# Kernel optimization log

Hardware: AMD Instinct MI355X
Metric: run time of the kernel (lower is better)

The kernel has to match this reference:

```python
import jax, jax.numpy as jnp
import numpy as np

WH, WW = 16, 16          # window size
S = WH * WW              # tokens per window = 256
B = 128                  # batch of windows
E = 1024                 # embed_dim
H = 16                   # num_heads
D = E // H               # head_dim = 64


def _swin_rel_index():
    # Swin-style relative position index, identical to the torch buffer construction
    coords = np.stack(np.meshgrid(np.arange(WH), np.arange(WW), indexing='ij'))  # [2,WH,WW]
    cf = coords.reshape(2, -1)                         # [2, S]
    rel = cf[:, :, None] - cf[:, None, :]              # [2, S, S]
    rel = rel.transpose(1, 2, 0).copy()                # [S, S, 2]
    rel[..., 0] += WH - 1
    rel[..., 1] += WW - 1
    rel[..., 0] *= 2 * WW - 1
    return rel.sum(-1).astype(np.int32)                # [S, S] in [0, (2WH-1)(2WW-1))


def setup_inputs() -> dict:
    key = jax.random.key(0)
    ks = jax.random.split(key, 6)
    x = jax.random.normal(ks[0], (B, S, E), dtype=jnp.float32)
    qkv_w = jax.random.normal(ks[1], (3 * E, E), dtype=jnp.float32) * 0.02
    qkv_b = jax.random.normal(ks[2], (3 * E,), dtype=jnp.float32) * 0.02
    out_w = jax.random.normal(ks[3], (E, E), dtype=jnp.float32) * 0.02
    out_b = jax.random.normal(ks[4], (E,), dtype=jnp.float32) * 0.02
    bias_table = jax.random.normal(ks[5], ((2 * WH - 1) * (2 * WW - 1), H), dtype=jnp.float32) * 0.02
    rel_index = jnp.asarray(_swin_rel_index())
    return {"x": x, "qkv_w": qkv_w, "qkv_b": qkv_b, "out_w": out_w,
            "out_b": out_b, "bias_table": bias_table, "rel_index": rel_index,
            "x_ignored_": 0, "x_ignored_1_": 0}


def reference(x, qkv_w, qkv_b, out_w, out_b, bias_table, rel_index, x_ignored_, x_ignored_1_):
    b, s, e = x.shape
    h = bias_table.shape[-1]
    d = e // h
    # fused QKV projection
    qkv = x @ qkv_w.T + qkv_b                          # [b, s, 3e]
    qkv = qkv.reshape(b, s, 3, h, d)
    q, k, v = qkv[:, :, 0], qkv[:, :, 1], qkv[:, :, 2]  # [b, s, h, d]
    scale = d ** -0.5
    # learned relative position bias, [h, s, s]
    bias = bias_table[rel_index.reshape(-1)].reshape(s, s, h).transpose(2, 0, 1)
    scores = jnp.einsum('bqhd,bkhd->bhqk', q, k) * scale + bias[None]
    attn = jax.nn.softmax(scores, axis=-1)
    ctx = jnp.einsum('bhqk,bkhd->bqhd', attn, v).reshape(b, s, e)
    return ctx @ out_w.T + out_b
```

## Files before the change

kernel.cpp:

```cpp
#include <hip/hip_runtime.h>
#include <stdint.h>

#define BB 128
#define SS 256
#define EE 1024
#define HH 16
#define DD 64
#define MM (BB*SS)

#define LOG2E 1.44269504088896f

typedef __attribute__((ext_vector_type(8))) short bf16x8;
typedef __attribute__((ext_vector_type(4))) float f32x4;

__device__ __forceinline__ unsigned short f2bf(float f) {
  union { float f; unsigned int u; } c; c.f = f;
  unsigned int u = c.u;
  u += 0x7fffu + ((u >> 16) & 1u);
  return (unsigned short)(u >> 16);
}

__device__ __forceinline__ float fast_exp2(float x) {
#if __has_builtin(__builtin_amdgcn_exp2f)
  return __builtin_amdgcn_exp2f(x);
#else
  return exp2f(x);
#endif
}

__device__ __forceinline__ float fast_rcp(float x) {
#if __has_builtin(__builtin_amdgcn_rcpf)
  return __builtin_amdgcn_rcpf(x);
#else
  return 1.0f / x;
#endif
}

__device__ __forceinline__ void gld16(const unsigned short* g, unsigned short* l) {
  __builtin_amdgcn_global_load_lds((__attribute__((address_space(1))) void*)(g),
                                   (__attribute__((address_space(3))) void*)(l), 16, 0, 0);
}

__global__ __launch_bounds__(256) void prep_kernel(const float4* __restrict__ x4,
                                                   const float4* __restrict__ qw,
                                                   const float4* __restrict__ ow,
                                                   const float* __restrict__ btab,
                                                   const int* __restrict__ ridx,
                                                   ushort4* __restrict__ xb,
                                                   ushort4* __restrict__ qwb,
                                                   ushort4* __restrict__ owb,
                                                   float* __restrict__ biasC) {
  const int NX = (MM * EE) / 4;
  const int NQ = (3 * EE * EE) / 4;
  const int NO = (EE * EE) / 4;
  const int NBIAS = HH * SS * SS;
  const int total = NX + NQ + NO + NBIAS;
  int stride = gridDim.x * blockDim.x;
  for (int i = blockIdx.x * blockDim.x + threadIdx.x; i < total; i += stride) {
    if (i < NX) {
      float4 v = x4[i];
      ushort4 r; r.x = f2bf(v.x); r.y = f2bf(v.y); r.z = f2bf(v.z); r.w = f2bf(v.w);
      xb[i] = r;
    } else if (i < NX + NQ) {
      int t = i - NX;
      float4 v = qw[t];
      ushort4 r; r.x = f2bf(v.x); r.y = f2bf(v.y); r.z = f2bf(v.z); r.w = f2bf(v.w);
      qwb[t] = r;
    } else if (i < NX + NQ + NO) {
      int t = i - (NX + NQ);
      float4 v = ow[t];
      ushort4 r; r.x = f2bf(v.x); r.y = f2bf(v.y); r.z = f2bf(v.z); r.w = f2bf(v.w);
      owb[t] = r;
    } else {
      int t = i - (NX + NQ + NO);
      int h   = t >> 16;
      int row = (t >> 8) & 255;
      int lo  = (t >> 4) & 15;
      int hi  = t & 15;
      int col = hi * 16 + lo;
      biasC[t] = btab[ridx[row * SS + col] * HH + h] * LOG2E;
    }
  }
}

__device__ __forceinline__ void gemm_mainloop(const unsigned short* __restrict__ A,
                                              const unsigned short* __restrict__ Bw,
                                              unsigned short* As, unsigned short* Bs,
                                              int row0, int col0, int K,
                                              f32x4 acc[4][4]) {
  const int tid = threadIdx.x;
  const int wave = tid >> 6, lane = tid & 63;
  const int wm = wave & 1, wn = wave >> 1;
  const int l15 = lane & 15, quad = lane >> 4;
  const int ldrow = lane >> 2, ldc = lane & 3;
  const int gsw = (ldc ^ ((ldrow >> 1) & 3)) * 8;
  const int rsw = (l15 >> 1) & 3;
  const unsigned short* agp0 = A + (size_t)(row0 + wave * 16 + ldrow) * K + gsw;
  const unsigned short* agp1 = A + (size_t)(row0 + (4 + wave) * 16 + ldrow) * K + gsw;
  const unsigned short* bgp0 = Bw + (size_t)(col0 + wave * 16 + ldrow) * K + gsw;
  const unsigned short* bgp1 = Bw + (size_t)(col0 + (4 + wave) * 16 + ldrow) * K + gsw;
  unsigned short* al0 = As + wave * 512;
  unsigned short* al1 = As + (4 + wave) * 512;
  unsigned short* bl0 = Bs + wave * 512;
  unsigned short* bl1 = Bs + (4 + wave) * 512;
  for (int k0 = 0; k0 < K; k0 += 32) {
    gld16(agp0 + k0, al0);
    gld16(agp1 + k0, al1);
    gld16(bgp0 + k0, bl0);
    gld16(bgp1 + k0, bl1);
    __syncthreads();
    bf16x8 af[4], bfm[4];
#pragma unroll
    for (int i = 0; i < 4; ++i)
      af[i] = *(const bf16x8*)(As + (wm * 64 + i * 16 + l15) * 32 + (quad ^ rsw) * 8);
#pragma unroll
    for (int j = 0; j < 4; ++j)
      bfm[j] = *(const bf16x8*)(Bs + (wn * 64 + j * 16 + l15) * 32 + (quad ^ rsw) * 8);
#pragma unroll
    for (int i = 0; i < 4; ++i)
#pragma unroll
      for (int j = 0; j < 4; ++j)
        acc[i][j] = __builtin_amdgcn_mfma_f32_16x16x32_bf16(af[i], bfm[j], acc[i][j], 0, 0, 0);
    __syncthreads();
  }
}

__global__ __launch_bounds__(256) void qkv_gemm(const unsigned short* __restrict__ A,
                                                const unsigned short* __restrict__ Bw,
                                                const float* __restrict__ bias,
                                                unsigned short* __restrict__ q,
                                                unsigned short* __restrict__ kx,
                                                unsigned short* __restrict__ vt) {
  __shared__ unsigned short As[128 * 32];
  __shared__ unsigned short Bs[128 * 32];
  const int tid = threadIdx.x;
  const int wave = tid >> 6, lane = tid & 63;
  const int wm = wave & 1, wn = wave >> 1;
  const int l15 = lane & 15, quad = lane >> 4;
  const int row0 = blockIdx.x * 128;
  const int col0 = blockIdx.y * 128;
  f32x4 acc[4][4];
#pragma unroll
  for (int i = 0; i < 4; ++i)
#pragma unroll
    for (int j = 0; j < 4; ++j) acc[i][j] = (f32x4){0.f, 0.f, 0.f, 0.f};
  gemm_mainloop(A, Bw, As, Bs, row0, col0, EE, acc);
  const int which = col0 >> 10;
  const float QS = 0.125f * LOG2E;
#pragma unroll
  for (int i = 0; i < 4; ++i) {
    const int mbase = row0 + wm * 64 + i * 16 + quad * 4;
    const int bb = mbase >> 8;
    const int s0 = mbase & 255;
#pragma unroll
    for (int j = 0; j < 4; ++j) {
      const int n = col0 + wn * 64 + j * 16 + l15;
      const int hn = (n >> 6) & 15;
      const int d = n & 63;
      const float bv = bias[n];
      if (which == 0) {
        size_t base = ((size_t)(bb * HH + hn) * SS + s0) * DD + d;
#pragma unroll
        for (int r = 0; r < 4; ++r)
          q[base + (size_t)r * DD] = f2bf((acc[i][j][r] + bv) * QS);
      } else if (which == 1) {
        size_t base = ((size_t)(bb * HH + hn) * SS + s0) * DD + d;
#pragma unroll
        for (int r = 0; r < 4; ++r)
          kx[base + (size_t)r * DD] = f2bf(acc[i][j][r] + bv);
      } else {
        size_t base = ((size_t)(bb * HH + hn) * DD + d) * SS + s0;
        ushort4 pk;
        pk.x = f2bf(acc[i][j][0] + bv);
        pk.y = f2bf(acc[i][j][1] + bv);
        pk.z = f2bf(acc[i][j][2] + bv);
        pk.w = f2bf(acc[i][j][3] + bv);
        *(ushort4*)(vt + base) = pk;
      }
    }
  }
}

__global__ __launch_bounds__(256) void attn_kernel(const unsigned short* __restrict__ q,
                                                   const unsigned short* __restrict__ kx,
                                                   const unsigned short* __restrict__ vt,
                                                   const float* __restrict__ biasC,
                                                   unsigned short* __restrict__ ctx) {
  __shared__ unsigned short Ks[256 * 64];
  __shared__ unsigned short P[4][16 * 256];
  const int tid = threadIdx.x;
  const int wave = tid >> 6, lane = tid & 63;
  const int l15 = lane & 15, quad = lane >> 4;
  const int swl = l15 & 7;
  const int bh = blockIdx.x;
  const int h = bh & 15;
  const int b_ = bh >> 4;
  const unsigned short* qp = q + (size_t)bh * SS * DD;
  const unsigned short* kp = kx + (size_t)bh * SS * DD;
  const unsigned short* vp = vt + (size_t)bh * SS * DD;

#pragma unroll
  for (int rr = 0; rr < 8; ++rr) {
    int gc = rr * 256 + tid;
    int row = gc >> 3, sc = gc & 7;
    int c = sc ^ (row & 7);
    gld16(kp + row * 64 + c * 8, Ks + (rr * 256 + wave * 64) * 8);
  }
  __syncthreads();

  unsigned short* Pw = &P[wave][0];
  for (int qblk = 0; qblk < 4; ++qblk) {
    const int qr0 = qblk * 64 + wave * 16;
    bf16x8 aq0 = *(const bf16x8*)(qp + (qr0 + l15) * DD + quad * 8);
    bf16x8 aq1 = *(const bf16x8*)(qp + (qr0 + l15) * DD + 32 + quad * 8);

    f32x4 sacc[16];
#pragma unroll
    for (int j = 0; j < 16; ++j) sacc[j] = (f32x4){0.f, 0.f, 0.f, 0.f};
#pragma unroll
    for (int j = 0; j < 16; ++j) {
      const unsigned short* krow = Ks + (j * 16 + l15) * 64;
      bf16x8 b0 = *(const bf16x8*)(krow + (quad ^ swl) * 8);
      bf16x8 b1 = *(const bf16x8*)(krow + ((4 + quad) ^ swl) * 8);
      sacc[j] = __builtin_amdgcn_mfma_f32_16x16x32_bf16(aq0, b0, sacc[j], 0, 0, 0);
      sacc[j] = __builtin_amdgcn_mfma_f32_16x16x32_bf16(aq1, b1, sacc[j], 0, 0, 0);
    }
#pragma unroll
    for (int r = 0; r < 4; ++r) {
      const int prow = quad * 4 + r;
      const float* bC = biasC + ((size_t)((h * 256 + qr0 + prow) * 16 + l15)) * 16;
      float4 bv0 = ((const float4*)bC)[0];
      float4 bv1 = ((const float4*)bC)[1];
      float4 bv2 = ((const float4*)bC)[2];
      float4 bv3 = ((const float4*)bC)[3];
      float bj[16] = {bv0.x, bv0.y, bv0.z, bv0.w, bv1.x, bv1.y, bv1.z, bv1.w,
                      bv2.x, bv2.y, bv2.z, bv2.w, bv3.x, bv3.y, bv3.z, bv3.w};
      float s = 0.f;
#pragma unroll
      for (int j = 0; j < 16; ++j) {
        float e = fast_exp2(sacc[j][r] + bj[j]);
        sacc[j][r] = e;
        s += e;
      }
#pragma unroll
      for (int m = 8; m >= 1; m >>= 1) s += __shfl_xor(s, m, 16);
      float rs = fast_rcp(s);
      const int psw = prow & 7;
#pragma unroll
      for (int j = 0; j < 16; ++j) {
        union { float f; unsigned int u; } cv; cv.f = sacc[j][r] * rs;
        unsigned short pb = (unsigned short)((cv.u + 0x8000u) >> 16);
        Pw[prow * 256 + (((2 * j + (l15 >> 3)) ^ psw) << 3) + swl] = pb;
      }
    }
    f32x4 cacc[4];
#pragma unroll
    for (int nt = 0; nt < 4; ++nt) cacc[nt] = (f32x4){0.f, 0.f, 0.f, 0.f};
#pragma unroll
    for (int kk = 0; kk < 8; ++kk) {
      bf16x8 a = *(const bf16x8*)(Pw + l15 * 256 + (((kk * 4 + quad) ^ swl) << 3));
#pragma unroll
      for (int nt = 0; nt < 4; ++nt) {
        bf16x8 b = *(const bf16x8*)(vp + (nt * 16 + l15) * SS + kk * 32 + quad * 8);
        cacc[nt] = __builtin_amdgcn_mfma_f32_16x16x32_bf16(a, b, cacc[nt], 0, 0, 0);
      }
    }
#pragma unroll
    for (int nt = 0; nt < 4; ++nt)
#pragma unroll
      for (int r = 0; r < 4; ++r)
        ctx[(size_t)(b_ * SS + qr0 + quad * 4 + r) * EE + h * DD + nt * 16 + l15] =
            f2bf(cacc[nt][r]);
  }
}

__global__ __launch_bounds__(256) void out_gemm(const unsigned short* __restrict__ A,
                                                const unsigned short* __restrict__ Bw,
                                                const float* __restrict__ bias,
                                                float* __restrict__ out) {
  __shared__ unsigned short As[128 * 32];
  __shared__ unsigned short Bs[128 * 32];
  const int tid = threadIdx.x;
  const int wave = tid >> 6, lane = tid & 63;
  const int wm = wave & 1, wn = wave >> 1;
  const int l15 = lane & 15, quad = lane >> 4;
  const int row0 = blockIdx.x * 128;
  const int col0 = blockIdx.y * 128;
  f32x4 acc[4][4];
#pragma unroll
  for (int i = 0; i < 4; ++i)
#pragma unroll
    for (int j = 0; j < 4; ++j) acc[i][j] = (f32x4){0.f, 0.f, 0.f, 0.f};
  gemm_mainloop(A, Bw, As, Bs, row0, col0, EE, acc);
#pragma unroll
  for (int i = 0; i < 4; ++i) {
    const int m0 = row0 + wm * 64 + i * 16 + quad * 4;
#pragma unroll
    for (int j = 0; j < 4; ++j) {
      const int n = col0 + wn * 64 + j * 16 + l15;
      const float bv = bias[n];
#pragma unroll
      for (int r = 0; r < 4; ++r)
        out[(size_t)(m0 + r) * EE + n] = acc[i][j][r] + bv;
    }
  }
}

#define WS_XCTX  ((size_t)0)
#define WS_QKVW  ((size_t)67108864)
#define WS_OUTW  ((size_t)73400320)
#define WS_BIAS  ((size_t)75497472)
#define WS_Q     ((size_t)79691776)
#define WS_K     ((size_t)146800640)
#define WS_VT    ((size_t)213909504)

extern "C" void kernel_launch(void* const* d_in, const int* in_sizes, int n_in,
                              void* d_out, int out_size, void* d_ws, size_t ws_size,
                              hipStream_t stream) {
  (void)in_sizes; (void)n_in; (void)out_size; (void)ws_size;
  const float* x      = (const float*)d_in[0];
  const float* qkv_w  = (const float*)d_in[1];
  const float* qkv_b  = (const float*)d_in[2];
  const float* out_w  = (const float*)d_in[3];
  const float* out_b  = (const float*)d_in[4];
  const float* btab   = (const float*)d_in[5];
  const int*   ridx   = (const int*)d_in[6];
  float* out = (float*)d_out;
  char* ws = (char*)d_ws;

  unsigned short* xctx  = (unsigned short*)(ws + WS_XCTX);
  unsigned short* qkvwb = (unsigned short*)(ws + WS_QKVW);
  unsigned short* outwb = (unsigned short*)(ws + WS_OUTW);
  float*          biasC = (float*)(ws + WS_BIAS);
  unsigned short* q     = (unsigned short*)(ws + WS_Q);
  unsigned short* k     = (unsigned short*)(ws + WS_K);
  unsigned short* vt    = (unsigned short*)(ws + WS_VT);

  prep_kernel<<<8192, 256, 0, stream>>>((const float4*)x, (const float4*)qkv_w,
                                        (const float4*)out_w, btab, ridx,
                                        (ushort4*)xctx, (ushort4*)qkvwb,
                                        (ushort4*)outwb, biasC);
  qkv_gemm<<<dim3(MM / 128, (3 * EE) / 128), 256, 0, stream>>>(xctx, qkvwb, qkv_b,
                                                               q, k, vt);
  attn_kernel<<<BB * HH, 256, 0, stream>>>(q, k, vt, biasC, xctx);
  out_gemm<<<dim3(MM / 128, EE / 128), 256, 0, stream>>>(xctx, outwb, out_b, out);
}
```

Before: 785.6 us.

## Rewrite GEMMs with 256x256 tiles, double-buffered LDS pipeline and grid swizzle

```diff
diff --git a/kernel.cpp b/kernel.cpp
--- a/kernel.cpp
+++ b/kernel.cpp
@@ -83,98 +83,154 @@
   }
 }
 
-__device__ __forceinline__ void gemm_mainloop(const unsigned short* __restrict__ A,
-                                              const unsigned short* __restrict__ Bw,
-                                              unsigned short* As, unsigned short* Bs,
-                                              int row0, int col0, int K,
-                                              f32x4 acc[4][4]) {
+#define GEMM_NT 16
+
+__device__ __forceinline__ void mfma16(f32x4& c, bf16x8 a, bf16x8 b) {
+  c = __builtin_amdgcn_mfma_f32_16x16x32_bf16(a, b, c, 0, 0, 0);
+}
+
+#define STAGE_A(buf, kh, tt) do { \
+    unsigned short* _d = S_A + ((buf)*2 + (kh))*8192; \
+    gld16(srcA0 + (tt)*64 + (kh)*32, _d + ldso0); \
+    gld16(srcA1 + (tt)*64 + (kh)*32, _d + ldso1); } while (0)
+#define STAGE_B(buf, kh, tt) do { \
+    unsigned short* _d = S_B + ((buf)*2 + (kh))*8192; \
+    gld16(srcB0 + (tt)*64 + (kh)*32, _d + ldso0); \
+    gld16(srcB1 + (tt)*64 + (kh)*32, _d + ldso1); } while (0)
+#define LOAD_A8(buf, kh) do { \
+    const unsigned short* _u = S_A + ((buf)*2 + (kh))*8192 + aoff; \
+    _Pragma("unroll") for (int mi = 0; mi < 8; ++mi) \
+      af[mi] = *(const bf16x8*)(_u + mi*512); } while (0)
+#define LOAD_B2(buf, kh, nj0) do { \
+    const unsigned short* _u = S_B + ((buf)*2 + (kh))*8192 + boff; \
+    bfr[(nj0)]   = *(const bf16x8*)(_u + (nj0)*512); \
+    bfr[(nj0)+1] = *(const bf16x8*)(_u + ((nj0)+1)*512); } while (0)
+#define MFMA_Q(nj0) do { \
+    _Pragma("unroll") for (int mi = 0; mi < 8; ++mi) { \
+      mfma16(acc[mi][(nj0)],   af[mi], bfr[(nj0)]); \
+      mfma16(acc[mi][(nj0)+1], af[mi], bfr[(nj0)+1]); } } while (0)
+#define WAIT_LGKM0() do { asm volatile("s_waitcnt lgkmcnt(0)" ::: "memory"); \
+                          __builtin_amdgcn_sched_barrier(0); } while (0)
+
+__device__ __forceinline__ void gemm256_loop(const unsigned short* __restrict__ A,
+                                             const unsigned short* __restrict__ Bw,
+                                             unsigned short* S_A, unsigned short* S_B,
+                                             int row0, int col0, f32x4 (&acc)[8][4]) {
   const int tid = threadIdx.x;
   const int wave = tid >> 6, lane = tid & 63;
-  const int wm = wave & 1, wn = wave >> 1;
+  const int wm = wave >> 2, wn = wave & 3;
   const int l15 = lane & 15, quad = lane >> 4;
-  const int ldrow = lane >> 2, ldc = lane & 3;
-  const int gsw = (ldc ^ ((ldrow >> 1) & 3)) * 8;
-  const int rsw = (l15 >> 1) & 3;
-  const unsigned short* agp0 = A + (size_t)(row0 + wave * 16 + ldrow) * K + gsw;
-  const unsigned short* agp1 = A + (size_t)(row0 + (4 + wave) * 16 + ldrow) * K + gsw;
-  const unsigned short* bgp0 = Bw + (size_t)(col0 + wave * 16 + ldrow) * K + gsw;
-  const unsigned short* bgp1 = Bw + (size_t)(col0 + (4 + wave) * 16 + ldrow) * K + gsw;
-  unsigned short* al0 = As + wave * 512;
-  unsigned short* al1 = As + (4 + wave) * 512;
-  unsigned short* bl0 = Bs + wave * 512;
-  unsigned short* bl1 = Bs + (4 + wave) * 512;
-  for (int k0 = 0; k0 < K; k0 += 32) {
-    gld16(agp0 + k0, al0);
-    gld16(agp1 + k0, al1);
-    gld16(bgp0 + k0, bl0);
-    gld16(bgp1 + k0, bl1);
-    __syncthreads();
-    bf16x8 af[4], bfm[4];
-#pragma unroll
-    for (int i = 0; i < 4; ++i)
-      af[i] = *(const bf16x8*)(As + (wm * 64 + i * 16 + l15) * 32 + (quad ^ rsw) * 8);
-#pragma unroll
-    for (int j = 0; j < 4; ++j)
-      bfm[j] = *(const bf16x8*)(Bs + (wn * 64 + j * 16 + l15) * 32 + (quad ^ rsw) * 8);
-#pragma unroll
-    for (int i = 0; i < 4; ++i)
-#pragma unroll
-      for (int j = 0; j < 4; ++j)
-        acc[i][j] = __builtin_amdgcn_mfma_f32_16x16x32_bf16(af[i], bfm[j], acc[i][j], 0, 0, 0);
-    __syncthreads();
-  }
-}
-
-__global__ __launch_bounds__(256) void qkv_gemm(const unsigned short* __restrict__ A,
-                                                const unsigned short* __restrict__ Bw,
-                                                const float* __restrict__ bias,
-                                                unsigned short* __restrict__ q,
-                                                unsigned short* __restrict__ kx,
-                                                unsigned short* __restrict__ vt) {
-  __shared__ unsigned short As[128 * 32];
-  __shared__ unsigned short Bs[128 * 32];
+  const int cq = quad ^ ((l15 >> 1) & 3);
+  const int aoff = (wm * 128 + l15) * 32 + cq * 8;
+  const int boff = (wn * 64 + l15) * 32 + cq * 8;
+  const int r0g = tid >> 2, c0g = tid & 3;
+  const int gc = c0g ^ ((r0g >> 1) & 3);
+  const unsigned short* srcA0 = A  + (size_t)(row0 + r0g) * EE + gc * 8;
+  const unsigned short* srcA1 = A  + (size_t)(row0 + 128 + r0g) * EE + gc * 8;
+  const unsigned short* srcB0 = Bw + (size_t)(col0 + r0g) * EE + gc * 8;
+  const unsigned short* srcB1 = Bw + (size_t)(col0 + 128 + r0g) * EE + gc * 8;
+  const int ldso0 = wave * 512;
+  const int ldso1 = 4096 + wave * 512;
+
+  STAGE_A(0, 0, 0); STAGE_B(0, 0, 0); STAGE_A(0, 1, 0); STAGE_B(0, 1, 0);
+  STAGE_A(1, 0, 1); STAGE_B(1, 0, 1); STAGE_A(1, 1, 1);
+  asm volatile("s_waitcnt vmcnt(6)" ::: "memory");
+  __builtin_amdgcn_sched_barrier(0);
+  __builtin_amdgcn_s_barrier();
+
+  bf16x8 af[8], bfr[4];
+  for (int t = 0; t < GEMM_NT; ++t) {
+    const int d = t & 1;
+    LOAD_A8(d, 0); LOAD_B2(d, 0, 0);
+    if (t + 1 < GEMM_NT) STAGE_B(d ^ 1, 1, t + 1);
+    __builtin_amdgcn_s_barrier();
+    WAIT_LGKM0();
+    __builtin_amdgcn_s_setprio(1);
+    MFMA_Q(0);
+    __builtin_amdgcn_s_setprio(0);
+    __builtin_amdgcn_s_barrier();
+    LOAD_B2(d, 0, 2);
+    if (t + 2 < GEMM_NT) STAGE_A(d, 0, t + 2);
+    __builtin_amdgcn_s_barrier();
+    WAIT_LGKM0();
+    __builtin_amdgcn_s_setprio(1);
+    MFMA_Q(2);
+    __builtin_amdgcn_s_setprio(0);
+    __builtin_amdgcn_s_barrier();
+    LOAD_A8(d, 1); LOAD_B2(d, 1, 0);
+    if (t + 2 < GEMM_NT) STAGE_B(d, 0, t + 2);
+    __builtin_amdgcn_s_barrier();
+    WAIT_LGKM0();
+    __builtin_amdgcn_s_setprio(1);
+    MFMA_Q(0);
+    __builtin_amdgcn_s_setprio(0);
+    __builtin_amdgcn_s_barrier();
+    LOAD_B2(d, 1, 2);
+    if (t + 2 < GEMM_NT) STAGE_A(d, 1, t + 2);
+    if (t < GEMM_NT - 2) { asm volatile("s_waitcnt vmcnt(6)" ::: "memory"); }
+    else                 { asm volatile("s_waitcnt vmcnt(0)" ::: "memory"); }
+    __builtin_amdgcn_sched_barrier(0);
+    __builtin_amdgcn_s_barrier();
+    WAIT_LGKM0();
+    __builtin_amdgcn_s_setprio(1);
+    MFMA_Q(2);
+    __builtin_amdgcn_s_setprio(0);
+    __builtin_amdgcn_s_barrier();
+  }
+}
+
+__global__ __launch_bounds__(512, 2) void qkv_gemm(const unsigned short* __restrict__ A,
+                                                   const unsigned short* __restrict__ Bw,
+                                                   const float* __restrict__ bias,
+                                                   unsigned short* __restrict__ q,
+                                                   unsigned short* __restrict__ kx,
+                                                   unsigned short* __restrict__ vt) {
+  __shared__ unsigned short S_A[32768];
+  __shared__ unsigned short S_B[32768];
+  const int bid = blockIdx.x;
+  const int swz = (bid & 7) * (gridDim.x >> 3) + (bid >> 3);
+  const int row0 = (swz & 127) * 256;
+  const int col0 = (swz >> 7) * 256;
   const int tid = threadIdx.x;
   const int wave = tid >> 6, lane = tid & 63;
-  const int wm = wave & 1, wn = wave >> 1;
+  const int wm = wave >> 2, wn = wave & 3;
   const int l15 = lane & 15, quad = lane >> 4;
-  const int row0 = blockIdx.x * 128;
-  const int col0 = blockIdx.y * 128;
-  f32x4 acc[4][4];
-#pragma unroll
-  for (int i = 0; i < 4; ++i)
+  f32x4 acc[8][4];
+#pragma unroll
+  for (int i = 0; i < 8; ++i)
 #pragma unroll
     for (int j = 0; j < 4; ++j) acc[i][j] = (f32x4){0.f, 0.f, 0.f, 0.f};
-  gemm_mainloop(A, Bw, As, Bs, row0, col0, EE, acc);
+  gemm256_loop(A, Bw, S_A, S_B, row0, col0, acc);
   const int which = col0 >> 10;
   const float QS = 0.125f * LOG2E;
 #pragma unroll
-  for (int i = 0; i < 4; ++i) {
-    const int mbase = row0 + wm * 64 + i * 16 + quad * 4;
-    const int bb = mbase >> 8;
-    const int s0 = mbase & 255;
-#pragma unroll
-    for (int j = 0; j < 4; ++j) {
-      const int n = col0 + wn * 64 + j * 16 + l15;
+  for (int mi = 0; mi < 8; ++mi) {
+    const int m = row0 + wm * 128 + mi * 16 + quad * 4;
+    const int bb = m >> 8;
+    const int s0 = m & 255;
+#pragma unroll
+    for (int nj = 0; nj < 4; ++nj) {
+      const int n = col0 + wn * 64 + nj * 16 + l15;
       const int hn = (n >> 6) & 15;
-      const int d = n & 63;
+      const int dd2 = n & 63;
       const float bv = bias[n];
       if (which == 0) {
-        size_t base = ((size_t)(bb * HH + hn) * SS + s0) * DD + d;
+        size_t base = ((size_t)(bb * HH + hn) * SS + s0) * DD + dd2;
 #pragma unroll
         for (int r = 0; r < 4; ++r)
-          q[base + (size_t)r * DD] = f2bf((acc[i][j][r] + bv) * QS);
+          q[base + (size_t)r * DD] = f2bf((acc[mi][nj][r] + bv) * QS);
       } else if (which == 1) {
-        size_t base = ((size_t)(bb * HH + hn) * SS + s0) * DD + d;
+        size_t base = ((size_t)(bb * HH + hn) * SS + s0) * DD + dd2;
 #pragma unroll
         for (int r = 0; r < 4; ++r)
-          kx[base + (size_t)r * DD] = f2bf(acc[i][j][r] + bv);
+          kx[base + (size_t)r * DD] = f2bf(acc[mi][nj][r] + bv);
       } else {
-        size_t base = ((size_t)(bb * HH + hn) * DD + d) * SS + s0;
+        size_t base = ((size_t)(bb * HH + hn) * DD + dd2) * SS + s0;
         ushort4 pk;
-        pk.x = f2bf(acc[i][j][0] + bv);
-        pk.y = f2bf(acc[i][j][1] + bv);
-        pk.z = f2bf(acc[i][j][2] + bv);
-        pk.w = f2bf(acc[i][j][3] + bv);
+        pk.x = f2bf(acc[mi][nj][0] + bv);
+        pk.y = f2bf(acc[mi][nj][1] + bv);
+        pk.z = f2bf(acc[mi][nj][2] + bv);
+        pk.w = f2bf(acc[mi][nj][3] + bv);
         *(ushort4*)(vt + base) = pk;
       }
     }
@@ -274,34 +330,36 @@
   }
 }
 
-__global__ __launch_bounds__(256) void out_gemm(const unsigned short* __restrict__ A,
-                                                const unsigned short* __restrict__ Bw,
-                                                const float* __restrict__ bias,
-                                                float* __restrict__ out) {
-  __shared__ unsigned short As[128 * 32];
-  __shared__ unsigned short Bs[128 * 32];
+__global__ __launch_bounds__(512, 2) void out_gemm(const unsigned short* __restrict__ A,
+                                                   const unsigned short* __restrict__ Bw,
+                                                   const float* __restrict__ bias,
+                                                   float* __restrict__ out) {
+  __shared__ unsigned short S_A[32768];
+  __shared__ unsigned short S_B[32768];
+  const int bid = blockIdx.x;
+  const int swz = (bid & 7) * (gridDim.x >> 3) + (bid >> 3);
+  const int row0 = (swz & 127) * 256;
+  const int col0 = (swz >> 7) * 256;
   const int tid = threadIdx.x;
   const int wave = tid >> 6, lane = tid & 63;
-  const int wm = wave & 1, wn = wave >> 1;
+  const int wm = wave >> 2, wn = wave & 3;
   const int l15 = lane & 15, quad = lane >> 4;
-  const int row0 = blockIdx.x * 128;
-  const int col0 = blockIdx.y * 128;
-  f32x4 acc[4][4];
-#pragma unroll
-  for (int i = 0; i < 4; ++i)
+  f32x4 acc[8][4];
+#pragma unroll
+  for (int i = 0; i < 8; ++i)
 #pragma unroll
     for (int j = 0; j < 4; ++j) acc[i][j] = (f32x4){0.f, 0.f, 0.f, 0.f};
-  gemm_mainloop(A, Bw, As, Bs, row0, col0, EE, acc);
-#pragma unroll
-  for (int i = 0; i < 4; ++i) {
-    const int m0 = row0 + wm * 64 + i * 16 + quad * 4;
-#pragma unroll
-    for (int j = 0; j < 4; ++j) {
-      const int n = col0 + wn * 64 + j * 16 + l15;
+  gemm256_loop(A, Bw, S_A, S_B, row0, col0, acc);
+#pragma unroll
+  for (int mi = 0; mi < 8; ++mi) {
+    const int m0 = row0 + wm * 128 + mi * 16 + quad * 4;
+#pragma unroll
+    for (int nj = 0; nj < 4; ++nj) {
+      const int n = col0 + wn * 64 + nj * 16 + l15;
       const float bv = bias[n];
 #pragma unroll
       for (int r = 0; r < 4; ++r)
-        out[(size_t)(m0 + r) * EE + n] = acc[i][j][r] + bv;
+        out[(size_t)(m0 + r) * EE + n] = acc[mi][nj][r] + bv;
     }
   }
 }
@@ -340,8 +398,8 @@
                                         (const float4*)out_w, btab, ridx,
                                         (ushort4*)xctx, (ushort4*)qkvwb,
                                         (ushort4*)outwb, biasC);
-  qkv_gemm<<<dim3(MM / 128, (3 * EE) / 128), 256, 0, stream>>>(xctx, qkvwb, qkv_b,
-                                                               q, k, vt);
+  qkv_gemm<<<dim3((MM / 256) * ((3 * EE) / 256)), 512, 0, stream>>>(xctx, qkvwb, qkv_b,
+                                                                    q, k, vt);
   attn_kernel<<<BB * HH, 256, 0, stream>>>(q, k, vt, biasC, xctx);
-  out_gemm<<<dim3(MM / 128, EE / 128), 256, 0, stream>>>(xctx, outwb, out_b, out);
-}
+  out_gemm<<<dim3((MM / 256) * (EE / 256)), 512, 0, stream>>>(xctx, outwb, out_b, out);
+}
```

Result: no change. 777.1 us (-1.1%).
